# Optimization experiments

Hardware: AMD Instinct MI355X
Metric: run time of the kernel (lower is better)

Reference implementation:

```python
import jax, jax.numpy as jnp
import numpy as np

N = 100000   # nodes
E = 1600000  # edges (avg degree 16)
IN, HID, OUT = 128, 128, 40
EPS = 1e-5   # BatchNorm1d default eps


def _lin(k, fan_in, fan_out):
    # Glorot-ish init for the linear weights
    return jax.random.normal(k, (fan_in, fan_out), jnp.float32) / np.sqrt(fan_in).astype(np.float32)


def setup_inputs() -> dict:
    key = jax.random.key(0)
    ks = jax.random.split(key, 12)
    return {
        "x": jax.random.normal(ks[0], (N, IN), jnp.float32),
        "edge_src": jax.random.randint(ks[1], (E,), 0, N, jnp.int32),
        "edge_dst": jax.random.randint(ks[2], (E,), 0, N, jnp.int32),
        # layer 0 (SAGEConv in->hid): lin_l (with bias) on aggregated neighbors, lin_r (no bias) on root
        "W_l0": _lin(ks[3], IN, HID), "b_l0": jnp.zeros((HID,), jnp.float32), "W_r0": _lin(ks[4], IN, HID),
        "g0": jnp.ones((HID,), jnp.float32), "be0": jnp.zeros((HID,), jnp.float32),
        # layer 1 (SAGEConv hid->hid)
        "W_l1": _lin(ks[5], HID, HID), "b_l1": jnp.zeros((HID,), jnp.float32), "W_r1": _lin(ks[6], HID, HID),
        "g1": jnp.ones((HID,), jnp.float32), "be1": jnp.zeros((HID,), jnp.float32),
        # layer 2 (SAGEConv hid->out)
        "W_l2": _lin(ks[7], HID, OUT), "b_l2": jnp.zeros((OUT,), jnp.float32), "W_r2": _lin(ks[8], HID, OUT),
    }


def reference(x, edge_src, edge_dst,
              W_l0, b_l0, W_r0, g0, be0,
              W_l1, b_l1, W_r1, g1, be1,
              W_l2, b_l2, W_r2):
    deg = jax.ops.segment_sum(jnp.ones((E,), x.dtype), edge_dst, num_segments=N)
    inv_deg = 1.0 / jnp.maximum(deg, 1.0)  # [N]

    def sage_conv(h, Wl, bl, Wr):
        # mean aggregation of neighbor features (gather + scatter-add), then two linears
        agg = jax.ops.segment_sum(h[edge_src], edge_dst, num_segments=N) * inv_deg[:, None]
        return agg @ Wl + bl + h @ Wr

    def bn(h, g, b):
        # BatchNorm1d in training mode: batch statistics over the node dimension
        m = h.mean(axis=0)
        v = h.var(axis=0)
        return (h - m) * (g / jnp.sqrt(v + EPS)) + b

    h = jax.nn.relu(bn(sage_conv(x, W_l0, b_l0, W_r0), g0, be0))
    h = jax.nn.relu(bn(sage_conv(h, W_l1, b_l1, W_r1), g1, be1))
    h = sage_conv(h, W_l2, b_l2, W_r2)
    return jax.nn.log_softmax(h, axis=-1)
```

## Files before the change

kernel.cpp:

```cpp
#include <hip/hip_runtime.h>
#include <hip/hip_bf16.h>

#define NNODES 100000
#define NEDGES 1600000
#define CH 128
#define OUTC 40
#define BN_EPS 1e-5f

__global__ void k_deg(const int* __restrict__ dst, int* __restrict__ deg) {
    int e = blockIdx.x * blockDim.x + threadIdx.x;
    if (e < NEDGES) atomicAdd(&deg[dst[e]], 1);
}

__global__ void k_scan1(const int* __restrict__ deg, int* __restrict__ row_ptr,
                        int* __restrict__ blkSums, float* __restrict__ inv_deg) {
    __shared__ int sd[256];
    int base = blockIdx.x * 1024 + threadIdx.x * 4;
    int t[4];
#pragma unroll
    for (int j = 0; j < 4; ++j) {
        int i = base + j;
        t[j] = (i < NNODES) ? deg[i] : 0;
        if (i < NNODES) inv_deg[i] = 1.0f / fmaxf((float)t[j], 1.0f);
    }
    int tsum = t[0] + t[1] + t[2] + t[3];
    sd[threadIdx.x] = tsum;
    __syncthreads();
    for (int off = 1; off < 256; off <<= 1) {
        int v = (threadIdx.x >= off) ? sd[threadIdx.x - off] : 0;
        __syncthreads();
        sd[threadIdx.x] += v;
        __syncthreads();
    }
    int run = sd[threadIdx.x] - tsum;
#pragma unroll
    for (int j = 0; j < 4; ++j) {
        int i = base + j;
        if (i < NNODES) row_ptr[i] = run;
        run += t[j];
    }
    if (threadIdx.x == 255) blkSums[blockIdx.x] = sd[255];
}

__global__ void k_scan2(int* blkSums, int nb) {
    if (threadIdx.x == 0 && blockIdx.x == 0) {
        int run = 0;
        for (int b = 0; b < nb; ++b) { int v = blkSums[b]; blkSums[b] = run; run += v; }
    }
}

__global__ void k_scan3(int* __restrict__ row_ptr, int* __restrict__ cursor,
                        const int* __restrict__ blkSums) {
    int i = blockIdx.x * blockDim.x + threadIdx.x;
    if (i < NNODES) {
        int v = row_ptr[i] + blkSums[i >> 10];
        row_ptr[i] = v;
        cursor[i] = v;
    }
    if (i == 0) row_ptr[NNODES] = NEDGES;
}

__global__ void k_fill(const int* __restrict__ src, const int* __restrict__ dst,
                       int* __restrict__ cursor, int* __restrict__ sorted_src) {
    int e = blockIdx.x * blockDim.x + threadIdx.x;
    if (e < NEDGES) {
        int d = dst[e];
        int pos = atomicAdd(&cursor[d], 1);
        sorted_src[pos] = src[e];
    }
}

template <int NC, int WP, bool BN_A>
__global__ __launch_bounds__(256) void k_gemm2(
    const float* __restrict__ h,
    const float* __restrict__ Wl, const float* __restrict__ Wr,
    const float* __restrict__ bias,
    const float* __restrict__ bnscale, const float* __restrict__ bnshift,
    float* __restrict__ yl, float* __restrict__ yr) {
    constexpr int NG = (NC == 128) ? 2 : 1;
    constexpr int WSLOTS = NC / 4;
    __shared__ float A_lds[128 * 36];
    __shared__ float W_lds[32 * WP];
    int tid = threadIdx.x;
    int ty = tid >> 4, tx = tid & 15;
    int row0 = blockIdx.x * 128;

    for (int half = 0; half < 2; ++half) {
        const float* W = half ? Wr : Wl;
        float acc[8][NG * 4];
#pragma unroll
        for (int i = 0; i < 8; ++i)
#pragma unroll
            for (int j = 0; j < NG * 4; ++j) acc[i][j] = 0.f;

        for (int kc = 0; kc < CH; kc += 32) {
            __syncthreads();
#pragma unroll
            for (int q = 0; q < 4; ++q) {
                int r = (tid >> 3) + 32 * q;
                int c = (tid & 7) << 2;
                int gr = row0 + r;
                float4 v = make_float4(0.f, 0.f, 0.f, 0.f);
                if (gr < NNODES) v = *(const float4*)&h[(size_t)gr * CH + kc + c];
                if (BN_A) {
                    float4 s4 = *(const float4*)&bnscale[kc + c];
                    float4 h4 = *(const float4*)&bnshift[kc + c];
                    v.x = fmaxf(fmaf(v.x, s4.x, h4.x), 0.f);
                    v.y = fmaxf(fmaf(v.y, s4.y, h4.y), 0.f);
                    v.z = fmaxf(fmaf(v.z, s4.z, h4.z), 0.f);
                    v.w = fmaxf(fmaf(v.w, s4.w, h4.w), 0.f);
                }
                *(float4*)&A_lds[r * 36 + c] = v;
            }
            for (int idx = tid; idx < 32 * WSLOTS; idx += 256) {
                int k = idx / WSLOTS, s = idx - k * WSLOTS;
                *(float4*)&W_lds[k * WP + s * 4] = *(const float4*)&W[(size_t)(kc + k) * NC + s * 4];
            }
            __syncthreads();
#pragma unroll
            for (int k4 = 0; k4 < 32; k4 += 4) {
                float4 a4[8];
#pragma unroll
                for (int i = 0; i < 8; ++i)
                    a4[i] = *(const float4*)&A_lds[(ty + 16 * i) * 36 + k4];
#pragma unroll
                for (int kk = 0; kk < 4; ++kk) {
                    float4 w0 = *(const float4*)&W_lds[(k4 + kk) * WP + tx * 4];
                    float4 w1;
                    if (NG == 2) w1 = *(const float4*)&W_lds[(k4 + kk) * WP + 64 + tx * 4];
#pragma unroll
                    for (int i = 0; i < 8; ++i) {
                        float av = (&a4[i].x)[kk];
                        acc[i][0] = fmaf(av, w0.x, acc[i][0]);
                        acc[i][1] = fmaf(av, w0.y, acc[i][1]);
                        acc[i][2] = fmaf(av, w0.z, acc[i][2]);
                        acc[i][3] = fmaf(av, w0.w, acc[i][3]);
                        if (NG == 2) {
                            acc[i][4] = fmaf(av, w1.x, acc[i][4]);
                            acc[i][5] = fmaf(av, w1.y, acc[i][5]);
                            acc[i][6] = fmaf(av, w1.z, acc[i][6]);
                            acc[i][7] = fmaf(av, w1.w, acc[i][7]);
                        }
                    }
                }
            }
        }
        float* Y = half ? yr : yl;
        bool colok = (NC != 40) || (tx < 10);
        float4 b0 = make_float4(0.f, 0.f, 0.f, 0.f), b1 = b0;
        if (half == 1 && colok) {
            b0 = *(const float4*)&bias[tx * 4];
            if (NG == 2) b1 = *(const float4*)&bias[64 + tx * 4];
        }
#pragma unroll
        for (int i = 0; i < 8; ++i) {
            int gr = row0 + ty + 16 * i;
            if (gr >= NNODES || !colok) continue;
            float4 v0 = make_float4(acc[i][0] + b0.x, acc[i][1] + b0.y,
                                    acc[i][2] + b0.z, acc[i][3] + b0.w);
            *(float4*)&Y[(size_t)gr * NC + tx * 4] = v0;
            if (NG == 2) {
                float4 v1 = make_float4(acc[i][4] + b1.x, acc[i][5] + b1.y,
                                        acc[i][6] + b1.z, acc[i][7] + b1.w);
                *(float4*)&Y[(size_t)gr * NC + 64 + tx * 4] = v1;
            }
        }
    }
}

__global__ void k_combine128(const float* __restrict__ yl, const int* __restrict__ row_ptr,
                             const int* __restrict__ sorted_src, const float* __restrict__ inv_deg,
                             float* __restrict__ z) {
    int wave = threadIdx.x >> 6, lane = threadIdx.x & 63;
    int node = blockIdx.x * 4 + wave;
    if (node >= NNODES) return;
    int s0 = row_ptr[node], s1 = row_ptr[node + 1];
    const float2* Y = (const float2*)yl;
    float ax0 = 0.f, ay0 = 0.f, ax1 = 0.f, ay1 = 0.f;
    float ax2 = 0.f, ay2 = 0.f, ax3 = 0.f, ay3 = 0.f;
    int e = s0;
    for (; e + 4 <= s1; e += 4) {
        int i0 = sorted_src[e], i1 = sorted_src[e + 1];
        int i2 = sorted_src[e + 2], i3 = sorted_src[e + 3];
        float2 v0 = Y[(size_t)i0 * 64 + lane];
        float2 v1 = Y[(size_t)i1 * 64 + lane];
        float2 v2 = Y[(size_t)i2 * 64 + lane];
        float2 v3 = Y[(size_t)i3 * 64 + lane];
        ax0 += v0.x; ay0 += v0.y; ax1 += v1.x; ay1 += v1.y;
        ax2 += v2.x; ay2 += v2.y; ax3 += v3.x; ay3 += v3.y;
    }
    for (; e < s1; ++e) {
        int i = sorted_src[e];
        float2 v = Y[(size_t)i * 64 + lane];
        ax0 += v.x; ay0 += v.y;
    }
    float w = inv_deg[node];
    float2* Z = (float2*)z;
    float2 r = Z[(size_t)node * 64 + lane];
    r.x += (ax0 + ax1 + ax2 + ax3) * w;
    r.y += (ay0 + ay1 + ay2 + ay3) * w;
    Z[(size_t)node * 64 + lane] = r;
}

__global__ void k_combine40_lsm(const float* __restrict__ yl, const float* __restrict__ yr,
                                const int* __restrict__ row_ptr, const int* __restrict__ sorted_src,
                                const float* __restrict__ inv_deg, float* __restrict__ out) {
    int wave = threadIdx.x >> 6, lane = threadIdx.x & 63;
    int node = blockIdx.x * 4 + wave;
    if (node >= NNODES) return;
    bool act = lane < 20;
    int s0 = row_ptr[node], s1 = row_ptr[node + 1];
    float ax0 = 0.f, ay0 = 0.f, ax1 = 0.f, ay1 = 0.f;
    float ax2 = 0.f, ay2 = 0.f, ax3 = 0.f, ay3 = 0.f;
    int e = s0;
    for (; e + 4 <= s1; e += 4) {
        int i0 = sorted_src[e], i1 = sorted_src[e + 1];
        int i2 = sorted_src[e + 2], i3 = sorted_src[e + 3];
        if (act) {
            float2 v0 = *(const float2*)&yl[(size_t)i0 * OUTC + lane * 2];
            float2 v1 = *(const float2*)&yl[(size_t)i1 * OUTC + lane * 2];
            float2 v2 = *(const float2*)&yl[(size_t)i2 * OUTC + lane * 2];
            float2 v3 = *(const float2*)&yl[(size_t)i3 * OUTC + lane * 2];
            ax0 += v0.x; ay0 += v0.y; ax1 += v1.x; ay1 += v1.y;
            ax2 += v2.x; ay2 += v2.y; ax3 += v3.x; ay3 += v3.y;
        }
    }
    for (; e < s1; ++e) {
        int i = sorted_src[e];
        if (act) {
            float2 v = *(const float2*)&yl[(size_t)i * OUTC + lane * 2];
            ax0 += v.x; ay0 += v.y;
        }
    }
    float zx = 0.f, zy = 0.f;
    if (act) {
        float w = inv_deg[node];
        float2 r = *(const float2*)&yr[(size_t)node * OUTC + lane * 2];
        zx = (ax0 + ax1 + ax2 + ax3) * w + r.x;
        zy = (ay0 + ay1 + ay2 + ay3) * w + r.y;
    }
    float m = act ? fmaxf(zx, zy) : -INFINITY;
#pragma unroll
    for (int off = 1; off <= 16; off <<= 1) m = fmaxf(m, __shfl_xor(m, off));
    float se = act ? (expf(zx - m) + expf(zy - m)) : 0.f;
#pragma unroll
    for (int off = 1; off <= 16; off <<= 1) se += __shfl_xor(se, off);
    float lse = m + logf(se);
    if (act) {
        float2 o = make_float2(zx - lse, zy - lse);
        *(float2*)&out[(size_t)node * OUTC + lane * 2] = o;
    }
}

__global__ void k_stats(const float* __restrict__ h, float* __restrict__ sums) {
    __shared__ float ls[256], ls2[256];
    int c = threadIdx.x & 127;
    int half = threadIdx.x >> 7;
    float s = 0.f, s2 = 0.f;
    for (int r = blockIdx.x * 2 + half; r < NNODES; r += gridDim.x * 2) {
        float v = h[(size_t)r * CH + c];
        s += v; s2 += v * v;
    }
    ls[threadIdx.x] = s; ls2[threadIdx.x] = s2;
    __syncthreads();
    if (half == 0) {
        atomicAdd(&sums[c], ls[c] + ls[c + 128]);
        atomicAdd(&sums[CH + c], ls2[c] + ls2[c + 128]);
    }
}

__global__ void k_bn_finalize(const float* __restrict__ sums, const float* __restrict__ g,
                              const float* __restrict__ be, float* __restrict__ scale,
                              float* __restrict__ shift) {
    int c = threadIdx.x;
    if (c < CH) {
        float mean = sums[c] * (1.0f / NNODES);
        float var = sums[128 + c] * (1.0f / NNODES) - mean * mean;
        float sc = g[c] * rsqrtf(var + BN_EPS);
        scale[c] = sc;
        shift[c] = be[c] - mean * sc;
    }
}

extern "C" void kernel_launch(void* const* d_in, const int* in_sizes, int n_in,
                              void* d_out, int out_size, void* d_ws, size_t ws_size,
                              hipStream_t stream) {
    const float* x   = (const float*)d_in[0];
    const int* esrc  = (const int*)d_in[1];
    const int* edst  = (const int*)d_in[2];
    const float* W_l0 = (const float*)d_in[3];
    const float* b_l0 = (const float*)d_in[4];
    const float* W_r0 = (const float*)d_in[5];
    const float* g0   = (const float*)d_in[6];
    const float* be0  = (const float*)d_in[7];
    const float* W_l1 = (const float*)d_in[8];
    const float* b_l1 = (const float*)d_in[9];
    const float* W_r1 = (const float*)d_in[10];
    const float* g1   = (const float*)d_in[11];
    const float* be1  = (const float*)d_in[12];
    const float* W_l2 = (const float*)d_in[13];
    const float* b_l2 = (const float*)d_in[14];
    const float* W_r2 = (const float*)d_in[15];
    float* out = (float*)d_out;

    char* w = (char*)d_ws;
    size_t o = 0;
    auto nxt = [&](size_t b) { void* p = w + o; o = (o + b + 511) & ~(size_t)511; return p; };
    int* deg      = (int*)nxt((size_t)NNODES * 4);
    int* row_ptr  = (int*)nxt((size_t)(NNODES + 1) * 4);
    int* cursor   = (int*)nxt((size_t)NNODES * 4);
    float* invdeg = (float*)nxt((size_t)NNODES * 4);
    int* blkSums  = (int*)nxt(128 * 4);
    float* sums   = (float*)nxt(512 * 4);
    float* scsh   = (float*)nxt(512 * 4);
    int* sorted   = (int*)nxt((size_t)NEDGES * 4);
    float* ylbuf  = (float*)nxt((size_t)NNODES * CH * 4);
    float* zA     = (float*)nxt((size_t)NNODES * CH * 4);
    float* zB     = (float*)nxt((size_t)NNODES * CH * 4);
    float* sums0 = sums, *sums1 = sums + 256;
    float* scale0 = scsh, *shift0 = scsh + 128, *scale1 = scsh + 256, *shift1 = scsh + 384;

    hipMemsetAsync(deg, 0, (size_t)NNODES * 4, stream);
    hipMemsetAsync(sums, 0, 512 * 4, stream);

    const int EB = (NEDGES + 255) / 256;
    const int SCAN_B = (NNODES + 1023) / 1024;
    const int NB = (NNODES + 255) / 256;
    const int COMB_B = (NNODES + 3) / 4;
    const int GEMM_B = (NNODES + 127) / 128;

    k_deg<<<EB, 256, 0, stream>>>(edst, deg);
    k_scan1<<<SCAN_B, 256, 0, stream>>>(deg, row_ptr, blkSums, invdeg);
    k_scan2<<<1, 64, 0, stream>>>(blkSums, SCAN_B);
    k_scan3<<<NB, 256, 0, stream>>>(row_ptr, cursor, blkSums);
    k_fill<<<EB, 256, 0, stream>>>(esrc, edst, cursor, sorted);

    k_gemm2<128, 132, false><<<GEMM_B, 256, 0, stream>>>(
        x, W_l0, W_r0, b_l0, nullptr, nullptr, ylbuf, zA);
    k_combine128<<<COMB_B, 256, 0, stream>>>(ylbuf, row_ptr, sorted, invdeg, zA);
    k_stats<<<256, 256, 0, stream>>>(zA, sums0);
    k_bn_finalize<<<1, 128, 0, stream>>>(sums0, g0, be0, scale0, shift0);

    k_gemm2<128, 132, true><<<GEMM_B, 256, 0, stream>>>(
        zA, W_l1, W_r1, b_l1, scale0, shift0, ylbuf, zB);
    k_combine128<<<COMB_B, 256, 0, stream>>>(ylbuf, row_ptr, sorted, invdeg, zB);
    k_stats<<<256, 256, 0, stream>>>(zB, sums1);
    k_bn_finalize<<<1, 128, 0, stream>>>(sums1, g1, be1, scale1, shift1);

    k_gemm2<40, 64, true><<<GEMM_B, 256, 0, stream>>>(
        zB, W_l2, W_r2, b_l2, scale1, shift1, ylbuf, zA);
    k_combine40_lsm<<<COMB_B, 256, 0, stream>>>(ylbuf, zA, row_ptr, sorted, invdeg, out);
}
```

Measured before the change: 1.050 ms.

## Replace FP32 SIMT GEMMs with split-bf16 MFMA GEMMs and pre-split weights

Swaps the scalar FMA GEMM kernels for MFMA bf16 kernels that emulate fp32 accuracy by splitting each operand into hi and lo bf16 parts and issuing three MFMAs (hi*hi, lo*hi, hi*lo). A new prep kernel transposes and splits the weights into bf16 hi/lo once per call. Activations are split on the fly and stored in XOR-swizzled LDS to avoid bank conflicts. This targets the compute cost of the dense transforms. In exchange it uses large LDS tiles that allow one block per CU, does scalar output stores, and accepts a small accuracy loss from dropping the lo*lo term.

```diff
diff --git a/kernel.cpp b/kernel.cpp
--- a/kernel.cpp
+++ b/kernel.cpp
@@ -6,6 +6,17 @@
 #define CH 128
 #define OUTC 40
 #define BN_EPS 1e-5f
+
+typedef __attribute__((ext_vector_type(8))) short s8v;
+typedef __attribute__((ext_vector_type(4))) float f32x4;
+
+__device__ inline unsigned short f2bf_rn(float f) {
+    unsigned u = __float_as_uint(f);
+    return (unsigned short)((u + 0x7FFFu + ((u >> 16) & 1u)) >> 16);
+}
+__device__ inline float bf2f(unsigned short b) {
+    return __uint_as_float((unsigned)b << 16);
+}
 
 __global__ void k_deg(const int* __restrict__ dst, int* __restrict__ deg) {
     int e = blockIdx.x * blockDim.x + threadIdx.x;
@@ -70,99 +81,167 @@
     }
 }
 
-template <int NC, int WP, bool BN_A>
-__global__ __launch_bounds__(256) void k_gemm2(
-    const float* __restrict__ h,
-    const float* __restrict__ Wl, const float* __restrict__ Wr,
+__global__ void k_prepw(const float* __restrict__ Wl0, const float* __restrict__ Wr0,
+                        const float* __restrict__ Wl1, const float* __restrict__ Wr1,
+                        const float* __restrict__ Wl2, const float* __restrict__ Wr2,
+                        short* __restrict__ wt) {
+    int gid = blockIdx.x * 256 + threadIdx.x;
+    const float* W;
+    int col, k, base, halfsz;
+    float val;
+    if (gid < 65536) {
+        int w = gid >> 14;
+        int r = gid & 16383;
+        col = r >> 7; k = r & 127;
+        W = (w == 0) ? Wl0 : (w == 1) ? Wr0 : (w == 2) ? Wl1 : Wr1;
+        val = W[k * 128 + col];
+        base = w * 32768; halfsz = 16384;
+    } else if (gid < 77824) {
+        int r2 = gid - 65536;
+        int w = r2 / 6144;
+        int r = r2 - w * 6144;
+        col = r >> 7; k = r & 127;
+        W = w ? Wr2 : Wl2;
+        val = (col < OUTC) ? W[k * OUTC + col] : 0.f;
+        base = 131072 + w * 12288; halfsz = 6144;
+    } else {
+        return;
+    }
+    unsigned short hi = f2bf_rn(val);
+    unsigned short lo = f2bf_rn(val - bf2f(hi));
+    int idx = col * 128 + k;
+    wt[base + idx] = (short)hi;
+    wt[base + halfsz + idx] = (short)lo;
+}
+
+template <int WRW, int WCW, int RF, int CF, int WCOLS, int NCR, int LSZ, bool BN_A>
+__global__ __launch_bounds__(256, 1) void k_gemm_mfma(
+    const float* __restrict__ H,
+    const short* __restrict__ WtL, const short* __restrict__ WtR,
     const float* __restrict__ bias,
     const float* __restrict__ bnscale, const float* __restrict__ bnshift,
     float* __restrict__ yl, float* __restrict__ yr) {
-    constexpr int NG = (NC == 128) ? 2 : 1;
-    constexpr int WSLOTS = NC / 4;
-    __shared__ float A_lds[128 * 36];
-    __shared__ float W_lds[32 * WP];
+    __shared__ short A_hi[128 * 128];
+    __shared__ short A_lo[128 * 128];
+    __shared__ short B_hi[WCOLS * 128];
+    __shared__ short B_lo[WCOLS * 128];
+
     int tid = threadIdx.x;
-    int ty = tid >> 4, tx = tid & 15;
     int row0 = blockIdx.x * 128;
 
+#pragma unroll
+    for (int i = 0; i < 8; ++i) {
+        int c = tid + 256 * i;
+        int r = c >> 4;
+        int k0 = (c & 15) << 3;
+        int gr = row0 + r;
+        float f[8];
+        if (gr < NNODES) {
+            float4 v0 = *(const float4*)&H[(size_t)gr * CH + k0];
+            float4 v1 = *(const float4*)&H[(size_t)gr * CH + k0 + 4];
+            f[0] = v0.x; f[1] = v0.y; f[2] = v0.z; f[3] = v0.w;
+            f[4] = v1.x; f[5] = v1.y; f[6] = v1.z; f[7] = v1.w;
+        } else {
+#pragma unroll
+            for (int j = 0; j < 8; ++j) f[j] = 0.f;
+        }
+        if (BN_A) {
+            float4 s0 = *(const float4*)&bnscale[k0];
+            float4 s1 = *(const float4*)&bnscale[k0 + 4];
+            float4 h0 = *(const float4*)&bnshift[k0];
+            float4 h1 = *(const float4*)&bnshift[k0 + 4];
+            f[0] = fmaxf(fmaf(f[0], s0.x, h0.x), 0.f);
+            f[1] = fmaxf(fmaf(f[1], s0.y, h0.y), 0.f);
+            f[2] = fmaxf(fmaf(f[2], s0.z, h0.z), 0.f);
+            f[3] = fmaxf(fmaf(f[3], s0.w, h0.w), 0.f);
+            f[4] = fmaxf(fmaf(f[4], s1.x, h1.x), 0.f);
+            f[5] = fmaxf(fmaf(f[5], s1.y, h1.y), 0.f);
+            f[6] = fmaxf(fmaf(f[6], s1.z, h1.z), 0.f);
+            f[7] = fmaxf(fmaf(f[7], s1.w, h1.w), 0.f);
+        }
+        s8v hi8, lo8;
+#pragma unroll
+        for (int j = 0; j < 8; ++j) {
+            unsigned short h = f2bf_rn(f[j]);
+            hi8[j] = (short)h;
+            lo8[j] = (short)f2bf_rn(f[j] - bf2f(h));
+        }
+        int e = ((r << 7) + k0) ^ ((r & 7) << 3);
+        *(s8v*)&A_hi[e] = hi8;
+        *(s8v*)&A_lo[e] = lo8;
+    }
+
+    int lane = tid & 63;
+    int wid = tid >> 6;
+    int wr = wid / WCW, wc = wid % WCW;
+    int l15 = lane & 15, kb = lane >> 4;
+    int rowbase = wr * RF * 16;
+    int colbase = wc * CF * 16;
+
     for (int half = 0; half < 2; ++half) {
-        const float* W = half ? Wr : Wl;
-        float acc[8][NG * 4];
-#pragma unroll
-        for (int i = 0; i < 8; ++i)
-#pragma unroll
-            for (int j = 0; j < NG * 4; ++j) acc[i][j] = 0.f;
-
-        for (int kc = 0; kc < CH; kc += 32) {
-            __syncthreads();
-#pragma unroll
-            for (int q = 0; q < 4; ++q) {
-                int r = (tid >> 3) + 32 * q;
-                int c = (tid & 7) << 2;
-                int gr = row0 + r;
-                float4 v = make_float4(0.f, 0.f, 0.f, 0.f);
-                if (gr < NNODES) v = *(const float4*)&h[(size_t)gr * CH + kc + c];
-                if (BN_A) {
-                    float4 s4 = *(const float4*)&bnscale[kc + c];
-                    float4 h4 = *(const float4*)&bnshift[kc + c];
-                    v.x = fmaxf(fmaf(v.x, s4.x, h4.x), 0.f);
-                    v.y = fmaxf(fmaf(v.y, s4.y, h4.y), 0.f);
-                    v.z = fmaxf(fmaf(v.z, s4.z, h4.z), 0.f);
-                    v.w = fmaxf(fmaf(v.w, s4.w, h4.w), 0.f);
-                }
-                *(float4*)&A_lds[r * 36 + c] = v;
+        if (half == 1) __syncthreads();
+        const short* Wt = half ? WtR : WtL;
+        constexpr int WCHUNK = WCOLS * 16;
+#pragma unroll
+        for (int i = 0; i < (WCHUNK + 255) / 256; ++i) {
+            int c = tid + 256 * i;
+            if (c < WCHUNK) {
+                int col = c >> 4;
+                int k0 = (c & 15) << 3;
+                s8v hi8 = *(const s8v*)&Wt[col * 128 + k0];
+                s8v lo8 = *(const s8v*)&Wt[LSZ + col * 128 + k0];
+                int e = ((col << 7) + k0) ^ ((col & 7) << 3);
+                *(s8v*)&B_hi[e] = hi8;
+                *(s8v*)&B_lo[e] = lo8;
             }
-            for (int idx = tid; idx < 32 * WSLOTS; idx += 256) {
-                int k = idx / WSLOTS, s = idx - k * WSLOTS;
-                *(float4*)&W_lds[k * WP + s * 4] = *(const float4*)&W[(size_t)(kc + k) * NC + s * 4];
+        }
+        __syncthreads();
+
+        f32x4 acc[RF][CF];
+#pragma unroll
+        for (int i = 0; i < RF; ++i)
+#pragma unroll
+            for (int j = 0; j < CF; ++j) acc[i][j] = (f32x4){0.f, 0.f, 0.f, 0.f};
+
+#pragma unroll
+        for (int ks = 0; ks < 4; ++ks) {
+            s8v ah[RF], al[RF];
+#pragma unroll
+            for (int rf = 0; rf < RF; ++rf) {
+                int r = rowbase + rf * 16 + l15;
+                int e = ((r << 7) + ks * 32 + (kb << 3)) ^ ((r & 7) << 3);
+                ah[rf] = *(const s8v*)&A_hi[e];
+                al[rf] = *(const s8v*)&A_lo[e];
             }
-            __syncthreads();
-#pragma unroll
-            for (int k4 = 0; k4 < 32; k4 += 4) {
-                float4 a4[8];
-#pragma unroll
-                for (int i = 0; i < 8; ++i)
-                    a4[i] = *(const float4*)&A_lds[(ty + 16 * i) * 36 + k4];
-#pragma unroll
-                for (int kk = 0; kk < 4; ++kk) {
-                    float4 w0 = *(const float4*)&W_lds[(k4 + kk) * WP + tx * 4];
-                    float4 w1;
-                    if (NG == 2) w1 = *(const float4*)&W_lds[(k4 + kk) * WP + 64 + tx * 4];
-#pragma unroll
-                    for (int i = 0; i < 8; ++i) {
-                        float av = (&a4[i].x)[kk];
-                        acc[i][0] = fmaf(av, w0.x, acc[i][0]);
-                        acc[i][1] = fmaf(av, w0.y, acc[i][1]);
-                        acc[i][2] = fmaf(av, w0.z, acc[i][2]);
-                        acc[i][3] = fmaf(av, w0.w, acc[i][3]);
-                        if (NG == 2) {
-                            acc[i][4] = fmaf(av, w1.x, acc[i][4]);
-                            acc[i][5] = fmaf(av, w1.y, acc[i][5]);
-                            acc[i][6] = fmaf(av, w1.z, acc[i][6]);
-                            acc[i][7] = fmaf(av, w1.w, acc[i][7]);
-                        }
-                    }
+#pragma unroll
+            for (int cf = 0; cf < CF; ++cf) {
+                int cc = colbase + cf * 16 + l15;
+                int e = ((cc << 7) + ks * 32 + (kb << 3)) ^ ((cc & 7) << 3);
+                s8v bh = *(const s8v*)&B_hi[e];
+                s8v bl = *(const s8v*)&B_lo[e];
+#pragma unroll
+                for (int rf = 0; rf < RF; ++rf) {
+                    acc[rf][cf] = __builtin_amdgcn_mfma_f32_16x16x32_bf16(ah[rf], bh, acc[rf][cf], 0, 0, 0);
+                    acc[rf][cf] = __builtin_amdgcn_mfma_f32_16x16x32_bf16(al[rf], bh, acc[rf][cf], 0, 0, 0);
+                    acc[rf][cf] = __builtin_amdgcn_mfma_f32_16x16x32_bf16(ah[rf], bl, acc[rf][cf], 0, 0, 0);
                 }
             }
         }
+
         float* Y = half ? yr : yl;
-        bool colok = (NC != 40) || (tx < 10);
-        float4 b0 = make_float4(0.f, 0.f, 0.f, 0.f), b1 = b0;
-        if (half == 1 && colok) {
-            b0 = *(const float4*)&bias[tx * 4];
-            if (NG == 2) b1 = *(const float4*)&bias[64 + tx * 4];
-        }
-#pragma unroll
-        for (int i = 0; i < 8; ++i) {
-            int gr = row0 + ty + 16 * i;
-            if (gr >= NNODES || !colok) continue;
-            float4 v0 = make_float4(acc[i][0] + b0.x, acc[i][1] + b0.y,
-                                    acc[i][2] + b0.z, acc[i][3] + b0.w);
-            *(float4*)&Y[(size_t)gr * NC + tx * 4] = v0;
-            if (NG == 2) {
-                float4 v1 = make_float4(acc[i][4] + b1.x, acc[i][5] + b1.y,
-                                        acc[i][6] + b1.z, acc[i][7] + b1.w);
-                *(float4*)&Y[(size_t)gr * NC + 64 + tx * 4] = v1;
+#pragma unroll
+        for (int cf = 0; cf < CF; ++cf) {
+            int gcol = colbase + cf * 16 + l15;
+            float bb = 0.f;
+            if (half == 1 && gcol < NCR) bb = bias[gcol];
+#pragma unroll
+            for (int rf = 0; rf < RF; ++rf) {
+#pragma unroll
+                for (int r = 0; r < 4; ++r) {
+                    int grow = row0 + rowbase + rf * 16 + (lane >> 4) * 4 + r;
+                    if (grow < NNODES && gcol < NCR)
+                        Y[(size_t)grow * NCR + gcol] = acc[rf][cf][r] + bb;
+                }
             }
         }
     }
@@ -313,6 +392,7 @@
     int* blkSums  = (int*)nxt(128 * 4);
     float* sums   = (float*)nxt(512 * 4);
     float* scsh   = (float*)nxt(512 * 4);
+    short* wtbuf  = (short*)nxt(155648 * 2);
     int* sorted   = (int*)nxt((size_t)NEDGES * 4);
     float* ylbuf  = (float*)nxt((size_t)NNODES * CH * 4);
     float* zA     = (float*)nxt((size_t)NNODES * CH * 4);
@@ -320,6 +400,13 @@
     float* sums0 = sums, *sums1 = sums + 256;
     float* scale0 = scsh, *shift0 = scsh + 128, *scale1 = scsh + 256, *shift1 = scsh + 384;
 
+    const short* wtL0 = wtbuf;
+    const short* wtR0 = wtbuf + 32768;
+    const short* wtL1 = wtbuf + 65536;
+    const short* wtR1 = wtbuf + 98304;
+    const short* wtL2 = wtbuf + 131072;
+    const short* wtR2 = wtbuf + 143360;
+
     hipMemsetAsync(deg, 0, (size_t)NNODES * 4, stream);
     hipMemsetAsync(sums, 0, 512 * 4, stream);
 
@@ -329,25 +416,26 @@
     const int COMB_B = (NNODES + 3) / 4;
     const int GEMM_B = (NNODES + 127) / 128;
 
+    k_prepw<<<304, 256, 0, stream>>>(W_l0, W_r0, W_l1, W_r1, W_l2, W_r2, wtbuf);
     k_deg<<<EB, 256, 0, stream>>>(edst, deg);
     k_scan1<<<SCAN_B, 256, 0, stream>>>(deg, row_ptr, blkSums, invdeg);
     k_scan2<<<1, 64, 0, stream>>>(blkSums, SCAN_B);
     k_scan3<<<NB, 256, 0, stream>>>(row_ptr, cursor, blkSums);
     k_fill<<<EB, 256, 0, stream>>>(esrc, edst, cursor, sorted);
 
-    k_gemm2<128, 132, false><<<GEMM_B, 256, 0, stream>>>(
-        x, W_l0, W_r0, b_l0, nullptr, nullptr, ylbuf, zA);
+    k_gemm_mfma<2, 2, 4, 4, 128, 128, 16384, false><<<GEMM_B, 256, 0, stream>>>(
+        x, wtL0, wtR0, b_l0, nullptr, nullptr, ylbuf, zA);
     k_combine128<<<COMB_B, 256, 0, stream>>>(ylbuf, row_ptr, sorted, invdeg, zA);
     k_stats<<<256, 256, 0, stream>>>(zA, sums0);
     k_bn_finalize<<<1, 128, 0, stream>>>(sums0, g0, be0, scale0, shift0);
 
-    k_gemm2<128, 132, true><<<GEMM_B, 256, 0, stream>>>(
-        zA, W_l1, W_r1, b_l1, scale0, shift0, ylbuf, zB);
+    k_gemm_mfma<2, 2, 4, 4, 128, 128, 16384, true><<<GEMM_B, 256, 0, stream>>>(
+        zA, wtL1, wtR1, b_l1, scale0, shift0, ylbuf, zB);
     k_combine128<<<COMB_B, 256, 0, stream>>>(ylbuf, row_ptr, sorted, invdeg, zB);
     k_stats<<<256, 256, 0, stream>>>(zB, sums1);
     k_bn_finalize<<<1, 128, 0, stream>>>(sums1, g1, be1, scale1, shift1);
 
-    k_gemm2<40, 64, true><<<GEMM_B, 256, 0, stream>>>(
-        zB, W_l2, W_r2, b_l2, scale1, shift1, ylbuf, zA);
+    k_gemm_mfma<4, 1, 2, 3, 48, 40, 6144, true><<<GEMM_B, 256, 0, stream>>>(
+        zB, wtL2, wtR2, b_l2, scale1, shift1, ylbuf, zA);
     k_combine40_lsm<<<COMB_B, 256, 0, stream>>>(ylbuf, zA, row_ptr, sorted, invdeg, out);
 }
```

Result: faster. 1.010 ms (-3.8%).
